# Performance work log

Hardware: AMD Instinct MI355X
Metric: run time of the kernel (lower is better)

The kernel has to match this reference:

```python
import jax, jax.numpy as jnp
import numpy as np

TAU = 1.0  # gumbel-softmax temperature (self.temperature)


def setup_inputs() -> dict:
    key = jax.random.key(0)
    k1, k2, k3 = jax.random.split(key, 3)
    B, N, D = 4, 1024, 64
    node_features = jax.random.normal(k1, (B, N, D), dtype=jnp.float32)
    # edge_predictor params: Linear(2D -> D), Linear(D -> 1); stored as [in, out]
    W1 = jax.random.normal(k2, (2 * D, D), dtype=jnp.float32) * (1.0 / np.sqrt(2 * D))
    b1 = jnp.zeros((D,), dtype=jnp.float32)
    W2 = jax.random.normal(k3, (D, 1), dtype=jnp.float32) * (1.0 / np.sqrt(D))
    b2 = jnp.zeros((1,), dtype=jnp.float32)
    return {"node_features": node_features, "W1": W1, "b1": b1, "W2": W2, "b2": b2}


def reference(node_features, W1, b1, W2, b2):
    B, N, D = node_features.shape
    # cat([f_i, f_j]) @ W1 == f_i @ W1[:D] + f_j @ W1[D:] -> avoid [B,N,N,2D] concat
    h_src = jnp.einsum('bnd,de->bne', node_features, W1[:D])  # [B,N,D]
    h_dst = jnp.einsum('bnd,de->bne', node_features, W1[D:])  # [B,N,D]
    hidden = jax.nn.relu(h_src[:, :, None, :] + h_dst[:, None, :, :] + b1)  # [B,N,N,D]
    edge_logits = jnp.einsum('bijd,do->bij', hidden, W2) + b2[0]  # [B,N,N]
    edge_logits = 0.5 * (edge_logits + jnp.swapaxes(edge_logits, 1, 2))
    # training branch: gumbel-softmax (hard, straight-through) over [logit, 0] pair
    paired = jnp.stack([edge_logits, jnp.zeros_like(edge_logits)], axis=-1)  # [B,N,N,2]
    g = jax.random.gumbel(jax.random.key(42), paired.shape, dtype=paired.dtype)
    y_soft = jax.nn.softmax((paired + g) / TAU, axis=-1)
    hard = jax.nn.one_hot(jnp.argmax(y_soft, axis=-1), 2, dtype=y_soft.dtype)
    y = hard + y_soft - jax.lax.stop_gradient(y_soft)  # straight-through
    adj = y[..., 0] * (1.0 - jnp.eye(N, dtype=y.dtype))
    return adj, edge_logits
```

## Files before the change

### kernel.cpp

```cpp
#include <hip/hip_runtime.h>
#include <stdint.h>
#include <math.h>

#define NB 4
#define NN 1024
#define ND 64
#define RP 65

__device__ double g_hs[NB * NN * ND];
__device__ double g_hd[NB * NN * ND];
__device__ double g_w2d[ND];

__device__ __forceinline__ void threefry_core(uint32_t K0, uint32_t K1,
                                              uint32_t x0, uint32_t x1,
                                              uint32_t& o0, uint32_t& o1) {
  const uint32_t K2 = K0 ^ K1 ^ 0x1BD11BDAu;
  x0 += K0; x1 += K1;
#define TF_RND(r) { x0 += x1; x1 = (x1 << r) | (x1 >> (32 - r)); x1 ^= x0; }
  TF_RND(13) TF_RND(15) TF_RND(26) TF_RND(6)
  x0 += K1; x1 += K2 + 1u;
  TF_RND(17) TF_RND(29) TF_RND(16) TF_RND(24)
  x0 += K2; x1 += K0 + 2u;
  TF_RND(13) TF_RND(15) TF_RND(26) TF_RND(6)
  x0 += K0; x1 += K1 + 3u;
  TF_RND(17) TF_RND(29) TF_RND(16) TF_RND(24)
  x0 += K1; x1 += K2 + 4u;
  TF_RND(13) TF_RND(15) TF_RND(26) TF_RND(6)
  x0 += K2; x1 += K0 + 5u;
#undef TF_RND
  o0 = x0; o1 = x1;
}

__device__ __forceinline__ uint32_t rand_word(uint32_t L) {
  uint32_t o0, o1;
  threefry_core(0u, 42u, 0u, L, o0, o1);
  return o0 ^ o1;
}

__device__ __forceinline__ double neglog_u(uint32_t idx) {
  uint32_t w = rand_word(idx);
  uint32_t fb = (w >> 9) | 0x3f800000u;
  float f = __uint_as_float(fb) - 1.0f;
  const float tinyf = 1.17549435e-38f;
  float u = fmaxf(tinyf, f + tinyf);
  return -log((double)u);
}

__global__ __launch_bounds__(256) void stage1(const float* __restrict__ nf,
                                              const float* __restrict__ W1,
                                              const float* __restrict__ b1,
                                              const float* __restrict__ W2) {
  __shared__ float w1s[2 * ND][ND];
  __shared__ float rows[4][ND];
  const int tid = threadIdx.x;
  const float4* W14 = (const float4*)W1;
  float4* w1s4 = (float4*)w1s;
  #pragma unroll
  for (int p = 0; p < 8; ++p) w1s4[tid + 256 * p] = W14[tid + 256 * p];
  const int r = tid >> 6, e = tid & 63;
  const int bn = blockIdx.x * 4 + r;
  rows[r][e] = nf[bn * ND + e];
  __syncthreads();
  double accs = 0.0, accd = 0.0;
  #pragma unroll
  for (int k = 0; k < ND; ++k) {
    double x = (double)rows[r][k];
    accs = fma(x, (double)w1s[k][e], accs);
    accd = fma(x, (double)w1s[ND + k][e], accd);
  }
  g_hs[bn * ND + e] = accs;
  g_hd[bn * ND + e] = accd + (double)b1[e];
  if (blockIdx.x == 0 && tid < ND) g_w2d[tid] = (double)W2[tid];
}

__global__ __launch_bounds__(256, 2) void stage2(const float* __restrict__ b2,
                                                 float* __restrict__ adj,
                                                 float* __restrict__ logits) {
  const int t = blockIdx.x;
  const int b = t / 528;
  const int k = t - b * 528;
#define TRI_S(x) ((x) * 32 - ((x) * ((x) - 1)) / 2)
  int bi = (int)((65.0 - sqrt((double)(4225 - 8 * k))) * 0.5);
  while (k >= TRI_S(bi + 1)) ++bi;
  while (k < TRI_S(bi)) --bi;
  const int bj = bi + (k - TRI_S(bi));
#undef TRI_S
  const int i0 = bi * 32, j0 = bj * 32;

  __shared__ double sh_si[32][RP], sh_di[32][RP];
  __shared__ double sh_sj[32][RP], sh_dj[32][RP];
  __shared__ double w2s[ND];

  const int tid = threadIdx.x;
  {
    const int c = tid & 63, rr = tid >> 6;
    #pragma unroll
    for (int p = 0; p < 8; ++p) {
      const int r = p * 4 + rr;
      const int gi = (b * NN + i0 + r) * ND + c;
      const int gj = (b * NN + j0 + r) * ND + c;
      sh_si[r][c] = g_hs[gi];
      sh_di[r][c] = g_hd[gi];
      sh_sj[r][c] = g_hs[gj];
      sh_dj[r][c] = g_hd[gj];
    }
    if (tid < ND) w2s[tid] = g_w2d[tid];
  }
  __syncthreads();

  const int tx = tid & 15, ty = tid >> 4;

  double a1[2][2] = {{0.0, 0.0}, {0.0, 0.0}};
  double a2[2][2] = {{0.0, 0.0}, {0.0, 0.0}};

  #pragma unroll 4
  for (int d = 0; d < ND; ++d) {
    const double w = w2s[d];
    double si[2], di[2], sj[2], dj[2];
    si[0] = sh_si[ty][d];      si[1] = sh_si[ty + 16][d];
    di[0] = sh_di[ty][d];      di[1] = sh_di[ty + 16][d];
    sj[0] = sh_sj[tx][d];      sj[1] = sh_sj[tx + 16][d];
    dj[0] = sh_dj[tx][d];      dj[1] = sh_dj[tx + 16][d];
    #pragma unroll
    for (int a = 0; a < 2; ++a)
      #pragma unroll
      for (int c = 0; c < 2; ++c) {
        a1[a][c] = fma(fmax(si[a] + dj[c], 0.0), w, a1[a][c]);
        a2[a][c] = fma(fmax(sj[c] + di[a], 0.0), w, a2[a][c]);
      }
  }

  const double b2d = (double)b2[0];

  #pragma unroll
  for (int a = 0; a < 2; ++a)
    #pragma unroll
    for (int c = 0; c < 2; ++c) {
      const int i = i0 + ty + 16 * a;
      const int j = j0 + tx + 16 * c;
      const double sym = 0.5 * (a1[a][c] + a2[a][c]) + b2d;
      const float symf = (float)sym;
      const double E = exp(sym);

      const uint32_t m1 = ((uint32_t)(b * NN + i)) * NN + (uint32_t)j;
      const uint32_t m2 = ((uint32_t)(b * NN + j)) * NN + (uint32_t)i;

      const double L0a = neglog_u(2u * m1), L1a = neglog_u(2u * m1 + 1u);
      const double L0b = neglog_u(2u * m2), L1b = neglog_u(2u * m2 + 1u);

      const float adj1 = (i == j) ? 0.0f : ((E * L1a >= L0a) ? 1.0f : 0.0f);
      const float adj2 = (i == j) ? 0.0f : ((E * L1b >= L0b) ? 1.0f : 0.0f);

      logits[m1] = symf;
      logits[m2] = symf;
      adj[m1] = adj1;
      adj[m2] = adj2;
    }
}

extern "C" void kernel_launch(void* const* d_in, const int* in_sizes, int n_in,
                              void* d_out, int out_size, void* d_ws, size_t ws_size,
                              hipStream_t stream) {
  const float* nf = (const float*)d_in[0];
  const float* W1 = (const float*)d_in[1];
  const float* b1 = (const float*)d_in[2];
  const float* W2 = (const float*)d_in[3];
  const float* b2 = (const float*)d_in[4];

  float* adj    = (float*)d_out;
  float* logits = adj + (size_t)NB * NN * NN;

  stage1<<<dim3(NB * NN / 4), dim3(256), 0, stream>>>(nf, W1, b1, W2);
  stage2<<<dim3(NB * 528), dim3(256), 0, stream>>>(b2, adj, logits);
}
```

Baseline: 160.8 us.

## Compute edge logits in fp32 with fp64 fallback for near-tie decisions

Switches the main pairwise MLP reduction and the Gumbel decision from double to float, using fast exp/log intrinsics and float4 shared-memory loads. Stage1 now writes both fp32 and fp64 copies of the projected features. When the float decision margin is within a small relative tolerance, a noinline fp64 fallback recomputes that edge from global memory. This cuts costly fp64 ALU work and halves LDS traffic and footprint, which allows a higher occupancy hint. The cost is extra stage1 writes, a divergent fallback path, and logits now produced in float precision.

```diff
diff --git a/kernel.cpp b/kernel.cpp
--- a/kernel.cpp
+++ b/kernel.cpp
@@ -5,11 +5,14 @@
 #define NB 4
 #define NN 1024
 #define ND 64
-#define RP 65
-
-__device__ double g_hs[NB * NN * ND];
-__device__ double g_hd[NB * NN * ND];
+#define RP 68
+
+__device__ double g_hs64[NB * NN * ND];
+__device__ double g_hd64[NB * NN * ND];
+__device__ float  g_hs32[NB * NN * ND];
+__device__ float  g_hd32[NB * NN * ND];
 __device__ double g_w2d[ND];
+__device__ float  g_w2f[ND];
 
 __device__ __forceinline__ void threefry_core(uint32_t K0, uint32_t K1,
                                               uint32_t x0, uint32_t x1,
@@ -37,13 +40,30 @@
   return o0 ^ o1;
 }
 
-__device__ __forceinline__ double neglog_u(uint32_t idx) {
-  uint32_t w = rand_word(idx);
+__device__ __forceinline__ float u_from_word(uint32_t w) {
   uint32_t fb = (w >> 9) | 0x3f800000u;
   float f = __uint_as_float(fb) - 1.0f;
   const float tinyf = 1.17549435e-38f;
-  float u = fmaxf(tinyf, f + tinyf);
-  return -log((double)u);
+  return fmaxf(tinyf, f + tinyf);
+}
+
+__device__ __attribute__((noinline)) float decide_fallback(int b, int i, int j,
+                                                           uint32_t m, double b2d) {
+  const double* hsi = g_hs64 + ((size_t)(b * NN + i)) * ND;
+  const double* hdi = g_hd64 + ((size_t)(b * NN + i)) * ND;
+  const double* hsj = g_hs64 + ((size_t)(b * NN + j)) * ND;
+  const double* hdj = g_hd64 + ((size_t)(b * NN + j)) * ND;
+  double l1 = 0.0, l2 = 0.0;
+  for (int d = 0; d < ND; ++d) {
+    double w = g_w2d[d];
+    l1 += fmax(hsi[d] + hdj[d], 0.0) * w;
+    l2 += fmax(hsj[d] + hdi[d], 0.0) * w;
+  }
+  double sym = 0.5 * (l1 + l2) + b2d;
+  double E = exp(sym);
+  double L0 = -log((double)u_from_word(rand_word(2u * m)));
+  double L1 = -log((double)u_from_word(rand_word(2u * m + 1u)));
+  return (E * L1 >= L0) ? 1.0f : 0.0f;
 }
 
 __global__ __launch_bounds__(256) void stage1(const float* __restrict__ nf,
@@ -68,12 +88,17 @@
     accs = fma(x, (double)w1s[k][e], accs);
     accd = fma(x, (double)w1s[ND + k][e], accd);
   }
-  g_hs[bn * ND + e] = accs;
-  g_hd[bn * ND + e] = accd + (double)b1[e];
-  if (blockIdx.x == 0 && tid < ND) g_w2d[tid] = (double)W2[tid];
-}
-
-__global__ __launch_bounds__(256, 2) void stage2(const float* __restrict__ b2,
+  accd += (double)b1[e];
+  const int o = bn * ND + e;
+  g_hs64[o] = accs;  g_hd64[o] = accd;
+  g_hs32[o] = (float)accs;  g_hd32[o] = (float)accd;
+  if (blockIdx.x == 0 && tid < ND) {
+    g_w2d[tid] = (double)W2[tid];
+    g_w2f[tid] = W2[tid];
+  }
+}
+
+__global__ __launch_bounds__(256, 4) void stage2(const float* __restrict__ b2,
                                                  float* __restrict__ adj,
                                                  float* __restrict__ logits) {
   const int t = blockIdx.x;
@@ -87,50 +112,61 @@
 #undef TRI_S
   const int i0 = bi * 32, j0 = bj * 32;
 
-  __shared__ double sh_si[32][RP], sh_di[32][RP];
-  __shared__ double sh_sj[32][RP], sh_dj[32][RP];
-  __shared__ double w2s[ND];
+  __shared__ float sh_si[32][RP], sh_di[32][RP];
+  __shared__ float sh_sj[32][RP], sh_dj[32][RP];
+  __shared__ float w2s[ND];
 
   const int tid = threadIdx.x;
   {
-    const int c = tid & 63, rr = tid >> 6;
+    const float4* src_si = (const float4*)(g_hs32 + ((size_t)(b * NN + i0)) * ND);
+    const float4* src_di = (const float4*)(g_hd32 + ((size_t)(b * NN + i0)) * ND);
+    const float4* src_sj = (const float4*)(g_hs32 + ((size_t)(b * NN + j0)) * ND);
+    const float4* src_dj = (const float4*)(g_hd32 + ((size_t)(b * NN + j0)) * ND);
     #pragma unroll
-    for (int p = 0; p < 8; ++p) {
-      const int r = p * 4 + rr;
-      const int gi = (b * NN + i0 + r) * ND + c;
-      const int gj = (b * NN + j0 + r) * ND + c;
-      sh_si[r][c] = g_hs[gi];
-      sh_di[r][c] = g_hd[gi];
-      sh_sj[r][c] = g_hs[gj];
-      sh_dj[r][c] = g_hd[gj];
+    for (int p = 0; p < 2; ++p) {
+      const int q = tid + 256 * p;
+      const int r = q >> 4, c4 = (q & 15) << 2;
+      *(float4*)&sh_si[r][c4] = src_si[q];
+      *(float4*)&sh_di[r][c4] = src_di[q];
+      *(float4*)&sh_sj[r][c4] = src_sj[q];
+      *(float4*)&sh_dj[r][c4] = src_dj[q];
     }
-    if (tid < ND) w2s[tid] = g_w2d[tid];
+    if (tid < ND) w2s[tid] = g_w2f[tid];
   }
   __syncthreads();
 
   const int tx = tid & 15, ty = tid >> 4;
 
-  double a1[2][2] = {{0.0, 0.0}, {0.0, 0.0}};
-  double a2[2][2] = {{0.0, 0.0}, {0.0, 0.0}};
+  float a1[2][2] = {{0.f, 0.f}, {0.f, 0.f}};
+  float a2[2][2] = {{0.f, 0.f}, {0.f, 0.f}};
 
   #pragma unroll 4
-  for (int d = 0; d < ND; ++d) {
-    const double w = w2s[d];
-    double si[2], di[2], sj[2], dj[2];
-    si[0] = sh_si[ty][d];      si[1] = sh_si[ty + 16][d];
-    di[0] = sh_di[ty][d];      di[1] = sh_di[ty + 16][d];
-    sj[0] = sh_sj[tx][d];      sj[1] = sh_sj[tx + 16][d];
-    dj[0] = sh_dj[tx][d];      dj[1] = sh_dj[tx + 16][d];
+  for (int d = 0; d < ND; d += 4) {
+    float wv[4], si[2][4], di[2][4], sj[2][4], dj[2][4];
+    *(float4*)wv    = *(const float4*)&w2s[d];
+    *(float4*)si[0] = *(const float4*)&sh_si[ty][d];
+    *(float4*)si[1] = *(const float4*)&sh_si[ty + 16][d];
+    *(float4*)di[0] = *(const float4*)&sh_di[ty][d];
+    *(float4*)di[1] = *(const float4*)&sh_di[ty + 16][d];
+    *(float4*)sj[0] = *(const float4*)&sh_sj[tx][d];
+    *(float4*)sj[1] = *(const float4*)&sh_sj[tx + 16][d];
+    *(float4*)dj[0] = *(const float4*)&sh_dj[tx][d];
+    *(float4*)dj[1] = *(const float4*)&sh_dj[tx + 16][d];
     #pragma unroll
-    for (int a = 0; a < 2; ++a)
+    for (int dd = 0; dd < 4; ++dd) {
+      const float w = wv[dd];
       #pragma unroll
-      for (int c = 0; c < 2; ++c) {
-        a1[a][c] = fma(fmax(si[a] + dj[c], 0.0), w, a1[a][c]);
-        a2[a][c] = fma(fmax(sj[c] + di[a], 0.0), w, a2[a][c]);
-      }
-  }
-
-  const double b2d = (double)b2[0];
+      for (int a = 0; a < 2; ++a)
+        #pragma unroll
+        for (int c = 0; c < 2; ++c) {
+          a1[a][c] = fmaf(fmaxf(si[a][dd] + dj[c][dd], 0.f), w, a1[a][c]);
+          a2[a][c] = fmaf(fmaxf(sj[c][dd] + di[a][dd], 0.f), w, a2[a][c]);
+        }
+    }
+  }
+
+  const float b2f = b2[0];
+  const double b2d = (double)b2f;
 
   #pragma unroll
   for (int a = 0; a < 2; ++a)
@@ -138,18 +174,27 @@
     for (int c = 0; c < 2; ++c) {
       const int i = i0 + ty + 16 * a;
       const int j = j0 + tx + 16 * c;
-      const double sym = 0.5 * (a1[a][c] + a2[a][c]) + b2d;
-      const float symf = (float)sym;
-      const double E = exp(sym);
-
-      const uint32_t m1 = ((uint32_t)(b * NN + i)) * NN + (uint32_t)j;
-      const uint32_t m2 = ((uint32_t)(b * NN + j)) * NN + (uint32_t)i;
-
-      const double L0a = neglog_u(2u * m1), L1a = neglog_u(2u * m1 + 1u);
-      const double L0b = neglog_u(2u * m2), L1b = neglog_u(2u * m2 + 1u);
-
-      const float adj1 = (i == j) ? 0.0f : ((E * L1a >= L0a) ? 1.0f : 0.0f);
-      const float adj2 = (i == j) ? 0.0f : ((E * L1b >= L0b) ? 1.0f : 0.0f);
+      const float symf = 0.5f * (a1[a][c] + a2[a][c]) + b2f;
+      const uint32_t m1 = (uint32_t)((b * NN + i) * NN + j);
+      const uint32_t m2 = (uint32_t)((b * NN + j) * NN + i);
+
+      const float E = __expf(symf);
+      const float L0a = -__logf(u_from_word(rand_word(2u * m1)));
+      const float L1a = -__logf(u_from_word(rand_word(2u * m1 + 1u)));
+      const float L0b = -__logf(u_from_word(rand_word(2u * m2)));
+      const float L1b = -__logf(u_from_word(rand_word(2u * m2 + 1u)));
+
+      float adj1, adj2;
+      if (i == j) {
+        adj1 = 0.f; adj2 = 0.f;
+      } else {
+        const float pa = E * L1a, da = pa - L0a;
+        const float pb = E * L1b, db = pb - L0b;
+        const bool flagA = (fabsf(da) < 2e-3f * (pa + L0a)) || ((pa + L0a) < 2e-6f);
+        const bool flagB = (fabsf(db) < 2e-3f * (pb + L0b)) || ((pb + L0b) < 2e-6f);
+        adj1 = flagA ? decide_fallback(b, i, j, m1, b2d) : (da >= 0.f ? 1.f : 0.f);
+        adj2 = flagB ? decide_fallback(b, i, j, m2, b2d) : (db >= 0.f ? 1.f : 0.f);
+      }
 
       logits[m1] = symf;
       logits[m2] = symf;
```

Measured after the change: 158.8 us. Within noise of the previous version (-1.2%).
